# Kernel tuning notes

Hardware: AMD Instinct MI355X
Metric: run time of the kernel (lower is better)

The kernel has to match this reference:

```python
import jax, jax.numpy as jnp
import numpy as np

V, A, D, H, M = 32000, 128, 256, 256, 256  # vocab, n_actions, emb, lstm hidden, mlp hidden
B, T = 64, 1024


def lstm_scan(xs, Wx, Wh, b):
    """xs: [T,B,D] -> hidden states [T,B,H] (zero initial state)."""
    Bsz = xs.shape[1]
    h0 = jnp.zeros((Bsz, Wh.shape[0]), xs.dtype)
    c0 = jnp.zeros_like(h0)

    def step(carry, x):
        h, c = carry
        g = x @ Wx + h @ Wh + b  # [B,4H]
        i, f, gg, o = jnp.split(g, 4, axis=-1)
        c = jax.nn.sigmoid(f) * c + jax.nn.sigmoid(i) * jnp.tanh(gg)
        h = jax.nn.sigmoid(o) * jnp.tanh(c)
        return (h, c), h

    _, hs = jax.lax.scan(step, (h0, c0), xs)
    return hs


def setup_inputs() -> dict:
    key = jax.random.key(0)
    ks = jax.random.split(key, 16)
    s = 0.05
    return {
        "stack_ids": jax.random.randint(ks[0], (B, T), 0, V),
        "buffer_ids": jax.random.randint(ks[1], (B, T), 0, V),
        "action_ids": jax.random.randint(ks[2], (B, T), 0, A),
        "word_emb": jax.random.normal(ks[3], (V, D), jnp.float32) * s,
        "action_emb": jax.random.normal(ks[4], (A, D), jnp.float32) * s,
        "Wsx": jax.random.normal(ks[5], (D, 4 * H), jnp.float32) * s,
        "Wsh": jax.random.normal(ks[6], (H, 4 * H), jnp.float32) * s,
        "bs": jnp.zeros((4 * H,), jnp.float32),
        "Whx": jax.random.normal(ks[7], (D, 4 * H), jnp.float32) * s,
        "Whh": jax.random.normal(ks[8], (H, 4 * H), jnp.float32) * s,
        "bh": jnp.zeros((4 * H,), jnp.float32),
        "W1": jax.random.normal(ks[9], (D + 2 * H, M), jnp.float32) * s,
        "b1": jnp.zeros((M,), jnp.float32),
        "W2": jax.random.normal(ks[10], (M, A), jnp.float32) * s,
        "b2": jnp.zeros((A,), jnp.float32),
    }


def reference(stack_ids, buffer_ids, action_ids, word_emb, action_emb,
              Wsx, Wsh, bs, Whx, Whh, bh, W1, b1, W2, b2):
    # Embedded per-step inputs (dropout p=0 -> identity)
    stack_x = word_emb[stack_ids]      # [B,T,D] items pushed on stack-LSTM
    buf = word_emb[buffer_ids]         # [B,T,D] buffer-top embedding at step t
    hist_x = action_emb[action_ids]    # [B,T,D] action taken at step t

    # Run the two recurrent encoders over time (scan over T, batched over B)
    s_hs = lstm_scan(stack_x.transpose(1, 0, 2), Wsx, Wsh, bs)  # [T,B,H]
    h_hs = lstm_scan(hist_x.transpose(1, 0, 2), Whx, Whh, bh)   # [T,B,H]

    # At step t the encoders have only seen items/actions from steps < t
    zero = jnp.zeros_like(s_hs[:1])
    s_t = jnp.concatenate([zero, s_hs[:-1]], 0).transpose(1, 0, 2)  # [B,T,H]
    h_t = jnp.concatenate([zero, h_hs[:-1]], 0).transpose(1, 0, 2)  # [B,T,H]

    x = jnp.concatenate([buf, h_t, s_t], axis=-1)  # [B,T,D+2H]
    logits = jax.nn.relu(x @ W1 + b1) @ W2 + b2    # [B,T,A]

    logp = jax.nn.log_softmax(logits, axis=-1)
    nll = -jnp.take_along_axis(logp, action_ids[..., None], axis=-1)[..., 0]
    return jnp.sum(nll)  # summed step losses, as in the original loop
```

## Files before the change

### kernel.cpp

```cpp
#include <hip/hip_runtime.h>
#include <stdint.h>

#define T_STEPS 1024
#define TC 128
#define NCHUNK (T_STEPS/TC)
#define ROLL (2*TC+1)
#define D_EMB 256
#define HID 256
#define VOCAB 32000
#define NACT 128
#define XDIM 768

typedef __attribute__((ext_vector_type(8))) short short8;
typedef __attribute__((ext_vector_type(4))) float f32x4;
typedef __attribute__((ext_vector_type(8))) int i32x8;
typedef unsigned short u16;
typedef unsigned int u32;
typedef unsigned char u8;

#define SGI (-1.4426950408889634f)
#define SGG ( 2.8853900817779268f)
#define KI (SGI/512.f)
#define KG (SGG/512.f)

#define HS 272
#define HB (16*HS)

__device__ __forceinline__ float bf2f(u16 u){
  union { u32 u; float f; } v; v.u = ((u32)u) << 16; return v.f;
}
__device__ __forceinline__ u16 f2bf(float f){
  union { float f; u32 u; } v; v.f = f;
  u32 u = v.u;
  return (u16)((u + 0x7FFFu + ((u >> 16) & 1u)) >> 16);
}
__device__ __forceinline__ void bf2x(u32 d, float& lo, float& hi){
  union { u32 u; float f; } a, b;
  a.u = d << 16; b.u = d & 0xffff0000u;
  lo = a.f; hi = b.f;
}
__device__ __forceinline__ float rcp_(float x){ return __builtin_amdgcn_rcpf(x); }
__device__ __forceinline__ float exp2_(float x){ return __builtin_amdgcn_exp2f(x); }
__device__ __forceinline__ ushort4 pack4(float4 v){
  ushort4 r; r.x=f2bf(v.x); r.y=f2bf(v.y); r.z=f2bf(v.z); r.w=f2bf(v.w); return r;
}
__device__ __forceinline__ u8 f2e4m3(float v){
  u32 p = __builtin_amdgcn_cvt_pk_fp8_f32(v, v, 0, false);
  return (u8)(p & 0xff);
}

__global__ void k_convert(const float* Wsx, const float* Wsh, const float* Whx, const float* Whh,
                          const float* W1, const float* W2,
                          u16* Wsxt, u16* Whxt, u8* Wsh8, u8* Whh8, u16* W1t, u16* W2t)
{
  const long NW = 1024L*256;
  const long NW1 = 256L*768;
  const long NW2 = 128L*256;
  const long total = 4*NW + NW1 + NW2;
  for (long i = blockIdx.x*(long)blockDim.x+threadIdx.x; i<total; i += (long)gridDim.x*blockDim.x){
    long j = i;
    if (j < NW){ long n=j>>8, k=j&255; Wsxt[j] = f2bf(Wsx[k*1024+n]); continue; } j -= NW;
    if (j < NW){ long n=j>>8, k=j&255; Whxt[j] = f2bf(Whx[k*1024+n]); continue; } j -= NW;
    if (j < NW){ long n=j>>8, k=j&255; Wsh8[j] = f2e4m3(Wsh[k*1024+n]*32.f); continue; } j -= NW;
    if (j < NW){ long n=j>>8, k=j&255; Whh8[j] = f2e4m3(Whh[k*1024+n]*32.f); continue; } j -= NW;
    if (j < NW1){ long n=j/768, k=j%768; float sc = (k>=256)?0.0625f:1.f;
                  W1t[j] = f2bf(W1[k*256+n]*sc); continue; } j -= NW1;
    { long n=j>>8, k=j&255; W2t[j] = f2bf(W2[k*128+n]); }
  }
}

__global__ __launch_bounds__(512) void k_fused(
    const int* stack_ids, const int* buffer_ids, const int* action_ids,
    const float* wemb, const float* aemb,
    const u16* Wsxt, const u16* Whxt, const float* bs_, const float* bh_,
    const u8* Wsh8, const u8* Whh8,
    const u16* gxcur_s, const u16* gxcur_h,
    u16* gxnext_s, u16* gxnext_h,
    u16* roll_s, u16* roll_h, float* cst,
    const u16* W1t, const float* b1, const u16* W2t, const float* b2, float* out,
    int rec_cs, int gx_cs, int mlp_cs)
{
  __shared__ __attribute__((aligned(16))) char arena[51456];
  const int bid = blockIdx.x;
  const int tid = threadIdx.x;
  const int wave = tid>>6, lane = tid&63, quad = lane>>4, l16 = lane&15;

  if (bid < 16){
    if (rec_cs < 0) return;
    __builtin_amdgcn_s_setprio(1);
    char* h8 = arena;
    const int lstm = bid>>3, bq = bid&7;
    const u8* Wh8 = lstm ? Whh8 : Wsh8;
    const u16* gxc = lstm ? gxcur_h : gxcur_s;
    u16* roll      = lstm ? roll_h : roll_s;
    const int w = wave;
    const int usub = quad>>1, rh = quad&1;
    const int rloc = rh*4;
    const int unit = w*32 + usub*16 + l16;
    float* cstp = cst + ((((size_t)lstm*8 + bq)*8 + w)*64 + lane)*4;

    i32x8 Bf8[8][2];
    #pragma unroll
    for (int ct=0; ct<8; ct++){
      int gate = ct & 3, usubB = ct >> 2;
      int col = gate*256 + w*32 + usubB*16 + l16;
      #pragma unroll
      for (int kh=0; kh<2; kh++){
        uint4* p = (uint4*)&Bf8[ct][kh];
        p[0] = *(const uint4*)(Wh8 + (size_t)col*256 + kh*128 + quad*32);
        p[1] = *(const uint4*)(Wh8 + (size_t)col*256 + kh*128 + quad*32 + 16);
      }
    }

    const size_t gxoff = (size_t)(bq>>1)*16384 + (size_t)unit*16 + (size_t)((bq&1)*8 + rloc);

    float c[4];
    if (rec_cs == 0){
      #pragma unroll
      for (int i=0;i<4;i++) c[i] = 0.f;
      for (int i = tid; i < HB/4; i += 512) ((int*)h8)[i] = 0;
    } else {
      float4 cv = *(const float4*)cstp;
      c[0]=cv.x; c[1]=cv.y; c[2]=cv.z; c[3]=cv.w;
      int slot = (rec_cs-1)%ROLL;
      #pragma unroll
      for (int i=0;i<4;i++){
        int idx = i*512 + tid; int row = idx>>8, un = idx&255;
        float hf = bf2f(roll[(size_t)slot*16384 + (bq*8+row)*256 + un]);
        char q8 = (char)f2e4m3(hf);
        h8[row*HS + un] = q8;
        h8[(row+8)*HS + un] = q8;
      }
    }
    __syncthreads();

    int par = 0;
    for (int tc=0; tc<TC; tc++){
      const int t = rec_cs + tc;
      const u16* gxt = gxc + (size_t)tc*65536 + gxoff;
      uint2 gxr[4];
      #pragma unroll
      for (int g=0; g<4; g++)
        gxr[g] = *(const uint2*)(gxt + (size_t)g*4096);
      f32x4 acc[8];
      #pragma unroll
      for (int ct=0;ct<8;ct++) acc[ct] = (f32x4)(0.f);
      #pragma unroll
      for (int kh=0;kh<2;kh++){
        i32x8 a;
        uint4* ap = (uint4*)&a;
        ap[0] = *(const uint4*)&h8[par*HB + l16*HS + kh*128 + quad*32];
        ap[1] = *(const uint4*)&h8[par*HB + l16*HS + kh*128 + quad*32 + 16];
        #pragma unroll
        for (int ct=0;ct<8;ct++)
          acc[ct] = __builtin_amdgcn_mfma_scale_f32_16x16x128_f8f6f4(
                      a, Bf8[ct][kh], acc[ct], 0, 0,
                      0, 0x7F7F7F7F, 0, 0x7F7F7F7F);
      }
      f32x4 aI = usub ? acc[4] : acc[0];
      f32x4 aF = usub ? acc[5] : acc[1];
      f32x4 aG = usub ? acc[6] : acc[2];
      f32x4 aO = usub ? acc[7] : acc[3];
      float gf_[4][4];
      #pragma unroll
      for (int g=0; g<4; g++){
        bf2x(gxr[g].x, gf_[g][0], gf_[g][1]);
        bf2x(gxr[g].y, gf_[g][2], gf_[g][3]);
      }
      float h16v[4];
      #pragma unroll
      for (int i2=0;i2<4;i2++){
        float argI = fmaf(aI[i2], KI, gf_[0][i2]);
        float argF = fmaf(aF[i2], KI, gf_[1][i2]);
        float argG = fmaf(aG[i2], KG, gf_[2][i2]);
        float argO = fmaf(aO[i2], KI, gf_[3][i2]);
        float eI = exp2_(argI), eF = exp2_(argF), eG = exp2_(argG), eO = exp2_(argO);
        float sF  = rcp_(1.f + eF);
        float rIG = rcp_((1.f + eI)*(1.f + eG));
        float cc  = sF*c[i2] + (eG - 1.f)*rIG;
        c[i2] = cc;
        float eC  = exp2_(cc * SGG);
        float num = fmaf(eC, 16.f, -16.f);
        float den = (1.f + eO)*(1.f + eC);
        h16v[i2] = num * rcp_(den);
      }
      const int slot_w = t % ROLL;
      u16* rbase = roll + (size_t)slot_w*16384 + (size_t)(bq*8 + rloc)*256 + unit;
      char* hbase = &h8[(par^1)*HB + rloc*HS + unit];
      #pragma unroll
      for (int p=0;p<2;p++){
        u32 pkb;
        asm("v_cvt_pk_bf16_f32 %0, %1, %2" : "=v"(pkb) : "v"(h16v[p*2]), "v"(h16v[p*2+1]));
        rbase[(p*2)*256]   = (u16)(pkb & 0xffff);
        rbase[(p*2+1)*256] = (u16)(pkb >> 16);
        u32 pk8 = __builtin_amdgcn_cvt_pk_fp8_f32(h16v[p*2], h16v[p*2+1], 0, false);
        char b0 = (char)(pk8 & 0xff), b1c = (char)((pk8 >> 8) & 0xff);
        hbase[(p*2)*HS]   = b0;
        hbase[(p*2+1)*HS] = b1c;
        hbase[(p*2+8)*HS] = b0;
        hbase[(p*2+9)*HS] = b1c;
      }
      __syncthreads();
      par ^= 1;
    }
    { float4 cv; cv.x=c[0]; cv.y=c[1]; cv.z=c[2]; cv.w=c[3]; *(float4*)cstp = cv; }

  } else if (bid < 272){
    if (gx_cs < 0) return;
    const int gid = bid - 16;
    const int tc = gid & 127, lstm = gid >> 7;
    const int t = gx_cs + tc;
    const int* ids = lstm ? action_ids : stack_ids;
    const float* emb = lstm ? aemb : wemb;
    const u16* Wxt = lstm ? Whxt : Wsxt;
    const float* bias = lstm ? bh_ : bs_;
    u16* gxc = (lstm ? gxnext_h : gxnext_s) + (size_t)tc*65536;
    u16* Ab = (u16*)arena;
    int* sids = (int*)(arena + 33792);

    if (tid < 64) sids[tid] = ids[tid*T_STEPS + t];
    __syncthreads();
    #pragma unroll
    for (int i=0;i<8;i++){
      int v = i*512 + tid; int b = v>>6, f0 = (v&63)*4;
      float4 ld = *(const float4*)(emb + (size_t)sids[b]*256 + f0);
      *(ushort4*)&Ab[b*264 + f0] = pack4(ld);
    }
    __syncthreads();

    for (int nc=0; nc<4; nc++){
      f32x4 acc[4][2];
      #pragma unroll
      for (int r=0;r<4;r++){ acc[r][0]=(f32x4)(0.f); acc[r][1]=(f32x4)(0.f); }
      #pragma unroll
      for (int kk=0;kk<8;kk++){
        short8 a[4], bfr[2];
        #pragma unroll
        for (int r=0;r<4;r++) a[r] = *(const short8*)&Ab[(r*16+l16)*264 + kk*32 + quad*8];
        #pragma unroll
        for (int cc=0;cc<2;cc++){
          int n = nc*256 + wave*32 + cc*16 + l16;
          bfr[cc] = *(const short8*)(Wxt + (size_t)n*256 + kk*32 + quad*8);
        }
        #pragma unroll
        for (int r=0;r<4;r++)
          #pragma unroll
          for (int cc=0;cc<2;cc++)
            acc[r][cc] = __builtin_amdgcn_mfma_f32_16x16x32_bf16(a[r], bfr[cc], acc[r][cc], 0,0,0);
      }
      #pragma unroll
      for (int cc=0;cc<2;cc++){
        int col = nc*256 + wave*32 + cc*16 + l16;
        float bv = bias[col];
        float sgm = ((col >> 8) == 2) ? SGG : SGI;
        #pragma unroll
        for (int r=0;r<4;r++){
          ushort4 o;
          o.x = f2bf((acc[r][cc][0]+bv)*sgm); o.y = f2bf((acc[r][cc][1]+bv)*sgm);
          o.z = f2bf((acc[r][cc][2]+bv)*sgm); o.w = f2bf((acc[r][cc][3]+bv)*sgm);
          *(ushort4*)&gxc[((size_t)r*1024 + col)*16 + quad*4] = o;
        }
      }
    }

  } else {
    if (mlp_cs < 0) return;
    const int t = mlp_cs + (bid - 272);
    u16* Axb = (u16*)arena;
    u16* lgb = (u16*)arena;
    u16* y1b = (u16*)(arena + 17408);
    int* sids = (int*)(arena + 51200);

    if (tid < 64) sids[tid] = buffer_ids[tid*T_STEPS + t];

    f32x4 acc1[2][4];
    #pragma unroll
    for (int nc=0;nc<2;nc++)
      #pragma unroll
      for (int r=0;r<4;r++) acc1[nc][r] = (f32x4)(0.f);

    for (int kc=0; kc<6; kc++){
      __syncthreads();
      if (kc < 2){
        #pragma unroll
        for (int i=0;i<4;i++){
          int v = i*512+tid; int b = v>>5, seg = v&31;
          float4 ld = *(const float4*)(wemb + (size_t)sids[b]*256 + kc*128 + seg*4);
          *(ushort4*)&Axb[b*136 + seg*4] = pack4(ld);
        }
      } else {
        const u16* roll = (kc < 4) ? roll_h : roll_s;
        int half = kc & 1;
        if (t == 0){
          uint4 z = make_uint4(0,0,0,0);
          #pragma unroll
          for (int i=0;i<2;i++){
            int v = i*512+tid; int b = v>>4, seg = v&15;
            *(uint4*)&Axb[b*136 + seg*8] = z;
          }
        } else {
          int slot = (t-1) % ROLL;
          #pragma unroll
          for (int i=0;i<2;i++){
            int v = i*512+tid; int b = v>>4, seg = v&15;
            *(uint4*)&Axb[b*136 + seg*8] =
              *(const uint4*)(roll + (size_t)slot*16384 + b*256 + half*128 + seg*8);
          }
        }
      }
      __syncthreads();
      #pragma unroll
      for (int nc=0;nc<2;nc++){
        int n = nc*128 + wave*16 + l16;
        #pragma unroll
        for (int kk=0;kk<4;kk++){
          short8 a[4];
          #pragma unroll
          for (int r=0;r<4;r++) a[r] = *(const short8*)&Axb[(r*16+l16)*136 + kk*32 + quad*8];
          short8 bb = *(const short8*)(W1t + (size_t)n*768 + kc*128 + kk*32 + quad*8);
          #pragma unroll
          for (int r=0;r<4;r++)
            acc1[nc][r] = __builtin_amdgcn_mfma_f32_16x16x32_bf16(a[r], bb, acc1[nc][r], 0,0,0);
        }
      }
    }
    #pragma unroll
    for (int nc=0;nc<2;nc++){
      int col = nc*128 + wave*16 + l16;
      float bv = b1[col];
      #pragma unroll
      for (int r=0;r<4;r++)
        #pragma unroll
        for (int i2=0;i2<4;i2++){
          int row = r*16 + quad*4 + i2;
          float y = acc1[nc][r][i2] + bv;
          y1b[row*264 + col] = f2bf(y > 0.f ? y : 0.f);
        }
    }
    __syncthreads();
    f32x4 acc2[4];
    #pragma unroll
    for (int r=0;r<4;r++) acc2[r] = (f32x4)(0.f);
    const int n2 = wave*16 + l16;
    #pragma unroll
    for (int kk=0;kk<8;kk++){
      short8 a[4];
      #pragma unroll
      for (int r=0;r<4;r++) a[r] = *(const short8*)&y1b[(r*16+l16)*264 + kk*32 + quad*8];
      short8 bb = *(const short8*)(W2t + (size_t)n2*256 + kk*32 + quad*8);
      #pragma unroll
      for (int r=0;r<4;r++)
        acc2[r] = __builtin_amdgcn_mfma_f32_16x16x32_bf16(a[r], bb, acc2[r], 0,0,0);
    }
    {
      float bv = b2[n2];
      #pragma unroll
      for (int r=0;r<4;r++)
        #pragma unroll
        for (int i2=0;i2<4;i2++)
          lgb[(r*16+quad*4+i2)*132 + n2] = f2bf(acc2[r][i2] + bv);
    }
    __syncthreads();
    if (tid < 64){
      int b = tid;
      float m = -1e30f;
      for (int j=0;j<128;j++) m = fmaxf(m, bf2f(lgb[b*132+j]));
      float s = 0.f;
      for (int j=0;j<128;j++) s += __expf(bf2f(lgb[b*132+j]) - m);
      int tgt = action_ids[b*T_STEPS + t];
      float v = __logf(s) + m - bf2f(lgb[b*132 + tgt]);
      #pragma unroll
      for (int o=32;o>0;o>>=1) v += __shfl_down(v, o);
      if (tid == 0) atomicAdd(out, v);
    }
  }
}

extern "C" void kernel_launch(void* const* d_in, const int* in_sizes, int n_in,
                              void* d_out, int out_size, void* d_ws, size_t ws_size,
                              hipStream_t stream)
{
  (void)in_sizes; (void)n_in; (void)out_size; (void)ws_size;
  const int* stack_ids  = (const int*)d_in[0];
  const int* buffer_ids = (const int*)d_in[1];
  const int* action_ids = (const int*)d_in[2];
  const float* word_emb   = (const float*)d_in[3];
  const float* action_emb = (const float*)d_in[4];
  const float* Wsx = (const float*)d_in[5];
  const float* Wsh = (const float*)d_in[6];
  const float* bs  = (const float*)d_in[7];
  const float* Whx = (const float*)d_in[8];
  const float* Whh = (const float*)d_in[9];
  const float* bh  = (const float*)d_in[10];
  const float* W1  = (const float*)d_in[11];
  const float* b1  = (const float*)d_in[12];
  const float* W2  = (const float*)d_in[13];
  const float* b2  = (const float*)d_in[14];
  float* out = (float*)d_out;

  char* ws = (char*)d_ws;
  size_t off = 0;
  auto alloc = [&](size_t bytes){ char* p = ws + off; off += (bytes + 255) & ~(size_t)255; return p; };
  u16* Wsxt = (u16*)alloc(1024*256*2);
  u16* Whxt = (u16*)alloc(1024*256*2);
  u8*  Wsh8 = (u8*)alloc(1024*256);
  u8*  Whh8 = (u8*)alloc(1024*256);
  u16* W1t  = (u16*)alloc(256*768*2);
  u16* W2t  = (u16*)alloc(128*256*2);
  u16* gxc_s[2], *gxc_h[2];
  gxc_s[0] = (u16*)alloc((size_t)TC*65536*2);
  gxc_s[1] = (u16*)alloc((size_t)TC*65536*2);
  gxc_h[0] = (u16*)alloc((size_t)TC*65536*2);
  gxc_h[1] = (u16*)alloc((size_t)TC*65536*2);
  u16* roll_s = (u16*)alloc((size_t)ROLL*64*256*2);
  u16* roll_h = (u16*)alloc((size_t)ROLL*64*256*2);
  float* cst  = (float*)alloc(2*8*8*64*4*4);

  (void)hipMemsetAsync(out, 0, sizeof(float), stream);
  k_convert<<<512, 256, 0, stream>>>(Wsx, Wsh, Whx, Whh, W1, W2,
                                     Wsxt, Whxt, Wsh8, Whh8, W1t, W2t);
  k_fused<<<400, 512, 0, stream>>>(stack_ids, buffer_ids, action_ids, word_emb, action_emb,
      Wsxt, Whxt, bs, bh, Wsh8, Whh8,
      gxc_s[0], gxc_h[0], gxc_s[0], gxc_h[0],
      roll_s, roll_h, cst, W1t, b1, W2t, b2, out,
      -1, 0, -1);
  for (int ch=0; ch<NCHUNK; ch++){
    int cs = ch*TC;
    int gx_cs  = (ch+1 < NCHUNK) ? (ch+1)*TC : -1;
    int mlp_cs = (ch > 0) ? (ch-1)*TC : -1;
    k_fused<<<400, 512, 0, stream>>>(stack_ids, buffer_ids, action_ids, word_emb, action_emb,
        Wsxt, Whxt, bs, bh, Wsh8, Whh8,
        gxc_s[ch&1], gxc_h[ch&1], gxc_s[(ch+1)&1], gxc_h[(ch+1)&1],
        roll_s, roll_h, cst, W1t, b1, W2t, b2, out,
        cs, gx_cs, mlp_cs);
  }
  k_fused<<<400, 512, 0, stream>>>(stack_ids, buffer_ids, action_ids, word_emb, action_emb,
      Wsxt, Whxt, bs, bh, Wsh8, Whh8,
      gxc_s[0], gxc_h[0], gxc_s[0], gxc_h[0],
      roll_s, roll_h, cst, W1t, b1, W2t, b2, out,
      -1, -1, (NCHUNK-1)*TC);
}
```

Baseline: 1.360 ms.

## Stage recurrent hidden outputs in LDS and flush to global every four steps

The recurrent blocks now write each step's bf16 hidden state into a double-buffered LDS staging area and, every four steps, copy the staged rows to the global roll buffer with wide 16-byte stores instead of scattered 2-byte global stores on the serial critical path. The fp8 h tile is also stored once (8 rows) rather than duplicated into 16 rows, with lanes reading rows via l16&7, which halves the LDS writes per step. This trades extra LDS traffic and a periodic flush step for fewer, coalesced global writes in the latency-bound recurrence.

Result: slower. 1.750 ms (+28.7%).

```diff
diff --git a/kernel.cpp b/kernel.cpp
--- a/kernel.cpp
+++ b/kernel.cpp
@@ -24,7 +24,7 @@
 #define KG (SGG/512.f)
 
 #define HS 272
-#define HB (16*HS)
+#define HB (8*HS)
 
 __device__ __forceinline__ float bf2f(u16 u){
   union { u32 u; float f; } v; v.u = ((u32)u) << 16; return v.f;
@@ -89,6 +89,7 @@
     if (rec_cs < 0) return;
     __builtin_amdgcn_s_setprio(1);
     char* h8 = arena;
+    u16* hstage = (u16*)(arena + 4352);
     const int lstm = bid>>3, bq = bid&7;
     const u8* Wh8 = lstm ? Whh8 : Wsh8;
     const u16* gxc = lstm ? gxcur_h : gxcur_s;
@@ -113,23 +114,26 @@
     }
 
     const size_t gxoff = (size_t)(bq>>1)*16384 + (size_t)unit*16 + (size_t)((bq&1)*8 + rloc);
+    const int fidx = tid*16;
+    const int fslot = fidx>>11, frow = (fidx>>8)&7, fcol = fidx&255;
 
     float c[4];
     if (rec_cs == 0){
       #pragma unroll
       for (int i=0;i<4;i++) c[i] = 0.f;
-      for (int i = tid; i < HB/4; i += 512) ((int*)h8)[i] = 0;
+      for (int i = tid; i < (2*HB)/4; i += 512) ((int*)h8)[i] = 0;
     } else {
       float4 cv = *(const float4*)cstp;
       c[0]=cv.x; c[1]=cv.y; c[2]=cv.z; c[3]=cv.w;
       int slot = (rec_cs-1)%ROLL;
-      #pragma unroll
-      for (int i=0;i<4;i++){
-        int idx = i*512 + tid; int row = idx>>8, un = idx&255;
-        float hf = bf2f(roll[(size_t)slot*16384 + (bq*8+row)*256 + un]);
-        char q8 = (char)f2e4m3(hf);
-        h8[row*HS + un] = q8;
-        h8[(row+8)*HS + un] = q8;
+      if (tid < 256){
+        int row = tid>>5, seg = tid&31;
+        #pragma unroll
+        for (int q=0;q<8;q++){
+          int un = seg*8+q;
+          float hf = bf2f(roll[(size_t)slot*16384 + (bq*8+row)*256 + un]);
+          h8[row*HS + un] = (char)f2e4m3(hf);
+        }
       }
     }
     __syncthreads();
@@ -142,6 +146,16 @@
       #pragma unroll
       for (int g=0; g<4; g++)
         gxr[g] = *(const uint2*)(gxt + (size_t)g*4096);
+      if (tc && (tc&3)==0){
+        int g = ((tc-4)>>2)&1;
+        const u16* src = hstage + g*8192 + fidx;
+        uint4 v0 = *(const uint4*)(src);
+        uint4 v1 = *(const uint4*)(src + 8);
+        int gslot = (rec_cs + tc-4 + fslot) % ROLL;
+        u16* dst = roll + (size_t)gslot*16384 + (size_t)(bq*8+frow)*256 + fcol;
+        *(uint4*)(dst)     = v0;
+        *(uint4*)(dst + 8) = v1;
+      }
       f32x4 acc[8];
       #pragma unroll
       for (int ct=0;ct<8;ct++) acc[ct] = (f32x4)(0.f);
@@ -149,8 +163,8 @@
       for (int kh=0;kh<2;kh++){
         i32x8 a;
         uint4* ap = (uint4*)&a;
-        ap[0] = *(const uint4*)&h8[par*HB + l16*HS + kh*128 + quad*32];
-        ap[1] = *(const uint4*)&h8[par*HB + l16*HS + kh*128 + quad*32 + 16];
+        ap[0] = *(const uint4*)&h8[par*HB + (l16&7)*HS + kh*128 + quad*32];
+        ap[1] = *(const uint4*)&h8[par*HB + (l16&7)*HS + kh*128 + quad*32 + 16];
         #pragma unroll
         for (int ct=0;ct<8;ct++)
           acc[ct] = __builtin_amdgcn_mfma_scale_f32_16x16x128_f8f6f4(
@@ -184,24 +198,30 @@
         float den = (1.f + eO)*(1.f + eC);
         h16v[i2] = num * rcp_(den);
       }
-      const int slot_w = t % ROLL;
-      u16* rbase = roll + (size_t)slot_w*16384 + (size_t)(bq*8 + rloc)*256 + unit;
+      u16* sbase = hstage + (((tc>>2)&1)*8192) + ((tc&3)*2048) + rloc*256 + unit;
       char* hbase = &h8[(par^1)*HB + rloc*HS + unit];
       #pragma unroll
       for (int p=0;p<2;p++){
         u32 pkb;
         asm("v_cvt_pk_bf16_f32 %0, %1, %2" : "=v"(pkb) : "v"(h16v[p*2]), "v"(h16v[p*2+1]));
-        rbase[(p*2)*256]   = (u16)(pkb & 0xffff);
-        rbase[(p*2+1)*256] = (u16)(pkb >> 16);
+        sbase[(p*2)*256]   = (u16)(pkb & 0xffff);
+        sbase[(p*2+1)*256] = (u16)(pkb >> 16);
         u32 pk8 = __builtin_amdgcn_cvt_pk_fp8_f32(h16v[p*2], h16v[p*2+1], 0, false);
-        char b0 = (char)(pk8 & 0xff), b1c = (char)((pk8 >> 8) & 0xff);
-        hbase[(p*2)*HS]   = b0;
-        hbase[(p*2+1)*HS] = b1c;
-        hbase[(p*2+8)*HS] = b0;
-        hbase[(p*2+9)*HS] = b1c;
+        hbase[(p*2)*HS]   = (char)(pk8 & 0xff);
+        hbase[(p*2+1)*HS] = (char)((pk8 >> 8) & 0xff);
       }
       __syncthreads();
       par ^= 1;
+    }
+    {
+      int g = ((TC-4)>>2)&1;
+      const u16* src = hstage + g*8192 + fidx;
+      uint4 v0 = *(const uint4*)(src);
+      uint4 v1 = *(const uint4*)(src + 8);
+      int gslot = (rec_cs + TC-4 + fslot) % ROLL;
+      u16* dst = roll + (size_t)gslot*16384 + (size_t)(bq*8+frow)*256 + fcol;
+      *(uint4*)(dst)     = v0;
+      *(uint4*)(dst + 8) = v1;
     }
     { float4 cv; cv.x=c[0]; cv.y=c[1]; cv.z=c[2]; cv.w=c[3]; *(float4*)cstp = cv; }
 
```
